# Optimization experiments

Measured on AMD Instinct MI355X. Metric: run time of the kernel, lower is better.

## Reference

```python
import jax, jax.numpy as jnp
import numpy as np

N_NODES = 100000


def _gcn_norm(edge_index, num_nodes):
    # add self loops, then symmetric normalization D^-1/2 (A+I) D^-1/2
    loops = jnp.arange(num_nodes, dtype=edge_index.dtype)
    src = jnp.concatenate([edge_index[0], loops])
    dst = jnp.concatenate([edge_index[1], loops])
    ones = jnp.ones(src.shape[0], dtype=jnp.float32)
    deg = jax.ops.segment_sum(ones, dst, num_segments=num_nodes)
    dinv = jnp.where(deg > 0, jax.lax.rsqrt(deg), 0.0)
    norm = dinv[src] * dinv[dst]  # [E+N]
    return src, dst, norm


def setup_inputs() -> dict:
    key = jax.random.key(0)
    k1, k2, k3, k4 = jax.random.split(key, 4)
    x = jax.random.normal(k1, (N_NODES, 512), dtype=jnp.float32)
    edge_index = jax.random.randint(k2, (2, 3200000), 0, N_NODES, dtype=jnp.int64)
    # SGConv linear: Linear(num_features=512, num_classes=40)
    W = jax.random.normal(k3, (40, 512), dtype=jnp.float32) / np.sqrt(512.0)
    b = jax.random.normal(k4, (40,), dtype=jnp.float32) * 0.01
    return {"x": x, "edge_index": edge_index, "W": W, "b": b}


def reference(x, edge_index, W, b):
    K = 2  # args.num_layers
    src, dst, norm = _gcn_norm(edge_index, N_NODES)
    h = x
    for _ in range(K):
        # SpMM: out[dst] += norm * h[src]
        h = jax.ops.segment_sum(norm[:, None] * h[src], dst, num_segments=N_NODES)
    logits = h @ W.T + b  # [N, num_classes]
    return jax.nn.log_softmax(logits, axis=1)
```

## Files before the change

### kernel.cpp

```cpp
#include <hip/hip_runtime.h>
#include <hip/hip_bf16.h>
#include <math.h>


#define NFEAT 512
#define NCLS  40
#define NBUCK_MAX 512
#define CAP   9728

typedef __attribute__((ext_vector_type(8))) short bf16x8;
typedef __attribute__((ext_vector_type(4))) float f32x4;

__device__ inline short f2bf(float f) {
    union { float f; unsigned u; } v; v.f = f;
    unsigned r = (v.u + 0x7FFFu + ((v.u >> 16) & 1u)) >> 16;
    return (short)r;
}
__device__ inline float bf2f(unsigned short u) {
    union { unsigned u; float f; } r; r.u = (unsigned)u << 16; return r.f;
}


__global__ __launch_bounds__(256) void scat7_kernel(const int* __restrict__ src,
                                                    const int* __restrict__ dst,
                                                    int* __restrict__ bcursor,
                                                    unsigned* __restrict__ bco, int E) {
    __shared__ int h[NBUCK_MAX], h2[NBUCK_MAX], base[NBUCK_MAX];
    int t = threadIdx.x;
    h[t] = 0; h[t + 256] = 0; h2[t] = 0; h2[t + 256] = 0;
    __syncthreads();
    int cb = blockIdx.x * 2048;
    int d[8], s[8];
    bool m[8];
    #pragma unroll
    for (int u = 0; u < 8; ++u) {
        int e = cb + u * 256 + t;
        m[u] = e < E;
        d[u] = m[u] ? __builtin_nontemporal_load(dst + e) : 0;
        s[u] = m[u] ? __builtin_nontemporal_load(src + e) : 0;
        if (m[u]) atomicAdd(&h[d[u] >> 8], 1);
    }
    __syncthreads();
    #pragma unroll
    for (int b = 0; b < 2; ++b) {
        int bb = t + b * 256;
        if (h[bb]) base[bb] = bb * CAP + atomicAdd(&bcursor[bb], h[bb]);
    }
    __syncthreads();
    #pragma unroll
    for (int u = 0; u < 8; ++u) {
        if (m[u]) {
            int b = d[u] >> 8;
            int lp = atomicAdd(&h2[b], 1);
            bco[base[b] + lp] = ((unsigned)s[u] << 8) | (unsigned)(d[u] & 255);
        }
    }
}


__global__ __launch_bounds__(256) void sortb3_kernel(const unsigned* __restrict__ bco,
                                                     const int* __restrict__ bcursor,
                                                     int4* __restrict__ rowinfo,
                                                     float* __restrict__ dinv,
                                                     int* __restrict__ csr_src, int N) {
    __shared__ int deg[256], ex[256], sc[256];
    int b = blockIdx.x, t = threadIdx.x;
    int lo = b * 256;
    int nn = N - lo; if (nn > 256) nn = 256;
    int ebeg = b * CAP;
    int ecnt = bcursor[b];

    deg[t] = 0;
    __syncthreads();
    for (int i = t; i < ecnt; i += 256)
        atomicAdd(&deg[bco[ebeg + i] & 255u], 1);
    __syncthreads();
    int v = deg[t];
    sc[t] = v;
    __syncthreads();
    for (int off = 1; off < 256; off <<= 1) {
        int u = (t >= off) ? sc[t - off] : 0;
        __syncthreads();
        sc[t] += u;
        __syncthreads();
    }
    int ext = sc[t] - v;
    ex[t] = ext;
    if (t < nn) {
        float di = rsqrtf((float)(v + 1));
        int4 ri;
        ri.x = ebeg + ext;
        ri.y = v;
        ri.z = __float_as_int(di);
        ri.w = 0;
        rowinfo[lo + t] = ri;
        dinv[lo + t]    = di;
    }
    __syncthreads();
    for (int i = t; i < ecnt; i += 256) {
        unsigned e = bco[ebeg + i];
        int p = atomicAdd(&ex[e & 255u], 1);
        csr_src[ebeg + p] = (int)(e >> 8);
    }
}


__global__ void wfrag_kernel(const float* __restrict__ W, short* __restrict__ wfrag) {
    int i = blockIdx.x * blockDim.x + threadIdx.x;
    if (i >= 16 * 3 * 64) return;
    int kc = i / 192, rem = i % 192, tile = rem / 64, lane = rem % 64;
    int c = tile * 16 + (lane & 15);
    int kbase = kc * 32 + ((lane >> 4) << 3);
    bf16x8 out;
    #pragma unroll
    for (int j = 0; j < 8; ++j) {
        float v = (c < NCLS) ? W[(size_t)c * NFEAT + kbase + j] : 0.f;
        out[j] = f2bf(v);
    }
    *(bf16x8*)(wfrag + (size_t)i * 8) = out;
}


__global__ __launch_bounds__(512) void gemm5_kernel(const float* __restrict__ x,
                                                    const short* __restrict__ wfrag,
                                                    const float* __restrict__ dinv,
                                                    unsigned short* __restrict__ zb, int n) {
    __shared__ short xl[2][128 * 40];
    int t = threadIdx.x;
    int w = t >> 6, l = t & 63;
    int lrow = l & 15, lk = l >> 4;
    int rowBase = blockIdx.x * 128;
    int srow = t >> 2, skq = t & 3;
    f32x4 acc0 = {0.f, 0.f, 0.f, 0.f}, acc1 = acc0, acc2 = acc0;
    const float* xrow = x + (size_t)(rowBase + srow) * NFEAT + skq * 8;
    bool srOK = (rowBase + srow) < n;
    int aoff = (w * 16 + lrow) * 40 + lk * 8;
    int doff = srow * 40 + skq * 8;

    {
        float4 v0 = make_float4(0.f, 0.f, 0.f, 0.f), v1 = v0;
        if (srOK) { const float4* xp = (const float4*)xrow; v0 = xp[0]; v1 = xp[1]; }
        bf16x8 bv;
        bv[0] = f2bf(v0.x); bv[1] = f2bf(v0.y); bv[2] = f2bf(v0.z); bv[3] = f2bf(v0.w);
        bv[4] = f2bf(v1.x); bv[5] = f2bf(v1.y); bv[6] = f2bf(v1.z); bv[7] = f2bf(v1.w);
        *(bf16x8*)&xl[0][doff] = bv;
    }
    __syncthreads();

    for (int kc = 0; kc < 16; ++kc) {
        int cur = kc & 1;
        float4 v0 = make_float4(0.f, 0.f, 0.f, 0.f), v1 = v0;
        if (kc < 15 && srOK) {
            const float4* xp = (const float4*)(xrow + (kc + 1) * 32);
            v0 = xp[0]; v1 = xp[1];
        }
        bf16x8 af = *(const bf16x8*)&xl[cur][aoff];
        const bf16x8* wf = (const bf16x8*)(wfrag + (size_t)kc * 3 * 64 * 8);
        bf16x8 b0 = wf[l];
        bf16x8 b1 = wf[64 + l];
        bf16x8 b2 = wf[128 + l];
        acc0 = __builtin_amdgcn_mfma_f32_16x16x32_bf16(af, b0, acc0, 0, 0, 0);
        acc1 = __builtin_amdgcn_mfma_f32_16x16x32_bf16(af, b1, acc1, 0, 0, 0);
        acc2 = __builtin_amdgcn_mfma_f32_16x16x32_bf16(af, b2, acc2, 0, 0, 0);
        if (kc < 15) {
            bf16x8 bv;
            bv[0] = f2bf(v0.x); bv[1] = f2bf(v0.y); bv[2] = f2bf(v0.z); bv[3] = f2bf(v0.w);
            bv[4] = f2bf(v1.x); bv[5] = f2bf(v1.y); bv[6] = f2bf(v1.z); bv[7] = f2bf(v1.w);
            *(bf16x8*)&xl[cur ^ 1][doff] = bv;
            __syncthreads();
        }
    }
    int r0 = rowBase + w * 16 + lk * 4;
    #pragma unroll
    for (int reg = 0; reg < 4; ++reg) {
        int row = r0 + reg;
        if (row < n) {
            float sc = dinv[row];
            unsigned short* zp = zb + (size_t)row * NCLS;
            zp[lrow]      = (unsigned short)f2bf(acc0[reg] * sc);
            zp[16 + lrow] = (unsigned short)f2bf(acc1[reg] * sc);
            if (lrow < 8) zp[32 + lrow] = (unsigned short)f2bf(acc2[reg] * sc);
        }
    }
}


template <bool FINAL>
__global__ __launch_bounds__(256) void spmm6_kernel(const unsigned short* __restrict__ in,
                                                    const int4* __restrict__ rowinfo,
                                                    const int* __restrict__ csr,
                                                    const float* __restrict__ bias,
                                                    void* __restrict__ outv, int n) {
    int wv = (int)((blockIdx.x * (size_t)blockDim.x + threadIdx.x) >> 6);
    wv = __builtin_amdgcn_readfirstlane(wv);
    if (wv >= n) return;
    int lane = threadIdx.x & 63;
    bool lact = lane < NCLS;

    int4 ri = rowinfo[wv];
    int beg = ri.x, tot = ri.y;
    float dd = __int_as_float(ri.z);

    float a = lact ? bf2f(in[(size_t)wv * NCLS + lane]) : 0.f;

    int j = 0;
    for (; j + 4 <= tot; j += 4) {
        int s0 = csr[beg + j];
        int s1 = csr[beg + j + 1];
        int s2 = csr[beg + j + 2];
        int s3 = csr[beg + j + 3];
        if (lact) {
            float v0 = bf2f(in[(size_t)s0 * NCLS + lane]);
            float v1 = bf2f(in[(size_t)s1 * NCLS + lane]);
            float v2 = bf2f(in[(size_t)s2 * NCLS + lane]);
            float v3 = bf2f(in[(size_t)s3 * NCLS + lane]);
            a += v0; a += v1; a += v2; a += v3;
        }
    }
    for (; j < tot; ++j) {
        int s = csr[beg + j];
        if (lact) a += bf2f(in[(size_t)s * NCLS + lane]);
    }

    if (!FINAL) {
        if (lact) {
            unsigned short* ob = (unsigned short*)outv;
            ob[(size_t)wv * NCLS + lane] = (unsigned short)f2bf(a * dd * dd);
        }
    } else {
        float v = lact ? a * dd + bias[lane] : -INFINITY;
        float m = v;
        #pragma unroll
        for (int off = 32; off; off >>= 1) m = fmaxf(m, __shfl_xor(m, off, 64));
        float e = lact ? expf(v - m) : 0.f;
        float s = e;
        #pragma unroll
        for (int off = 32; off; off >>= 1) s += __shfl_xor(s, off, 64);
        float lse = logf(s);
        if (lact) {
            float* out = (float*)outv;
            out[(size_t)wv * NCLS + lane] = v - m - lse;
        }
    }
}


extern "C" void kernel_launch(void* const* d_in, const int* in_sizes, int n_in,
                              void* d_out, int out_size, void* d_ws, size_t ws_size,
                              hipStream_t stream) {
    const float* x  = (const float*)d_in[0];
    const int*   ei = (const int*)d_in[1];
    const float* W  = (const float*)d_in[2];
    const float* b  = (const float*)d_in[3];

    const int N = in_sizes[0] / NFEAT;
    const int E = in_sizes[1] / 2;
    const int* src = ei;
    const int* dst = ei + E;
    const int nbuck = (N + 255) >> 8;

    char* p = (char*)d_ws;
    auto alloc = [&](size_t bytes) -> void* {
        void* r = (void*)p;
        p += (bytes + 255) & ~(size_t)255;
        return r;
    };
    int*      bcursor = (int*)     alloc((size_t)NBUCK_MAX * 4);
    int4*     rowinfo = (int4*)    alloc((size_t)N * 16);
    float*    dinv    = (float*)   alloc((size_t)N * 4);
    unsigned* bco     = (unsigned*)alloc((size_t)nbuck * CAP * 4 + 64);
    int*      csr_src = (int*)     alloc((size_t)nbuck * CAP * 4 + 64);
    short*    wfrag   = (short*)   alloc((size_t)16 * 3 * 64 * 8 * 2);
    unsigned short* zb = (unsigned short*)alloc((size_t)N * NCLS * 2 + 256);
    unsigned short* h1 = (unsigned short*)alloc((size_t)N * NCLS * 2 + 256);

    hipMemsetAsync(bcursor, 0, (size_t)NBUCK_MAX * 4, stream);

    int cb = (E + 2047) / 2048;
    scat7_kernel<<<cb, 256, 0, stream>>>(src, dst, bcursor, bco, E);
    sortb3_kernel<<<nbuck, 256, 0, stream>>>(bco, bcursor, rowinfo, dinv, csr_src, N);

    wfrag_kernel<<<12, 256, 0, stream>>>(W, wfrag);
    gemm5_kernel<<<(N + 127) / 128, 512, 0, stream>>>(x, wfrag, dinv, zb, N);

    int wb = (int)(((size_t)N * 64 + 255) / 256);
    spmm6_kernel<false><<<wb, 256, 0, stream>>>(zb, rowinfo, csr_src, b, h1, N);
    spmm6_kernel<true ><<<wb, 256, 0, stream>>>(h1, rowinfo, csr_src, b, d_out, N);
}
```

Baseline: 294.9 us.

## Pad features to 64 bf16 and gather 8 neighbors per wave with 16-byte loads

Intermediate feature rows are padded from 40 to 64 bf16 so that each row is 128 bytes. The SpMM kernel now assigns 8 lanes per neighbor row, each loading 16 bytes, so one wave gathers 8 neighbors at a time. Partial sums are combined with cross-lane shuffles and the log-softmax runs over packed lanes. The hipMemset is folded into the wfrag kernel, which now runs first. The change trades 60% more gather bytes from padding for fewer, wider memory transactions and more neighbors in flight per wave.

```diff
diff --git a/kernel.cpp b/kernel.cpp
--- a/kernel.cpp
+++ b/kernel.cpp
@@ -16,8 +16,14 @@
     unsigned r = (v.u + 0x7FFFu + ((v.u >> 16) & 1u)) >> 16;
     return (short)r;
 }
-__device__ inline float bf2f(unsigned short u) {
-    union { unsigned u; float f; } r; r.u = (unsigned)u << 16; return r.f;
+__device__ inline unsigned pack2bf(float a, float b) {
+    return (unsigned)(unsigned short)f2bf(a) | ((unsigned)(unsigned short)f2bf(b) << 16);
+}
+__device__ inline float bflo(unsigned v) {
+    union { unsigned u; float f; } r; r.u = v << 16; return r.f;
+}
+__device__ inline float bfhi(unsigned v) {
+    union { unsigned u; float f; } r; r.u = v & 0xFFFF0000u; return r.f;
 }
 
 
@@ -105,8 +111,10 @@
 }
 
 
-__global__ void wfrag_kernel(const float* __restrict__ W, short* __restrict__ wfrag) {
+__global__ void wfrag_kernel(const float* __restrict__ W, short* __restrict__ wfrag,
+                             int* __restrict__ bcursor) {
     int i = blockIdx.x * blockDim.x + threadIdx.x;
+    if (i < NBUCK_MAX) bcursor[i] = 0;
     if (i >= 16 * 3 * 64) return;
     int kc = i / 192, rem = i % 192, tile = rem / 64, lane = rem % 64;
     int c = tile * 16 + (lane & 15);
@@ -121,10 +129,10 @@
 }
 
 
-__global__ __launch_bounds__(512) void gemm5_kernel(const float* __restrict__ x,
+__global__ __launch_bounds__(512) void gemm7_kernel(const float* __restrict__ x,
                                                     const short* __restrict__ wfrag,
                                                     const float* __restrict__ dinv,
-                                                    unsigned short* __restrict__ zb, int n) {
+                                                    unsigned short* __restrict__ zp, int n) {
     __shared__ short xl[2][128 * 40];
     int t = threadIdx.x;
     int w = t >> 6, l = t & 63;
@@ -176,70 +184,123 @@
         int row = r0 + reg;
         if (row < n) {
             float sc = dinv[row];
-            unsigned short* zp = zb + (size_t)row * NCLS;
-            zp[lrow]      = (unsigned short)f2bf(acc0[reg] * sc);
-            zp[16 + lrow] = (unsigned short)f2bf(acc1[reg] * sc);
-            if (lrow < 8) zp[32 + lrow] = (unsigned short)f2bf(acc2[reg] * sc);
+            unsigned short* zr = zp + (size_t)row * 64;
+            zr[lrow]      = (unsigned short)f2bf(acc0[reg] * sc);
+            zr[16 + lrow] = (unsigned short)f2bf(acc1[reg] * sc);
+            zr[32 + lrow] = (lrow < 8) ? (unsigned short)f2bf(acc2[reg] * sc) : 0;
+            zr[48 + lrow] = 0;
         }
     }
 }
 
 
 template <bool FINAL>
-__global__ __launch_bounds__(256) void spmm6_kernel(const unsigned short* __restrict__ in,
-                                                    const int4* __restrict__ rowinfo,
-                                                    const int* __restrict__ csr,
-                                                    const float* __restrict__ bias,
-                                                    void* __restrict__ outv, int n) {
+__global__ __launch_bounds__(256) void spmm12_kernel(const unsigned short* __restrict__ in,
+                                                     const int4* __restrict__ rowinfo,
+                                                     const int* __restrict__ csr,
+                                                     const float* __restrict__ bias,
+                                                     unsigned short* __restrict__ outP,
+                                                     float* __restrict__ outF, int n) {
     int wv = (int)((blockIdx.x * (size_t)blockDim.x + threadIdx.x) >> 6);
     wv = __builtin_amdgcn_readfirstlane(wv);
     if (wv >= n) return;
     int lane = threadIdx.x & 63;
-    bool lact = lane < NCLS;
+    int g  = lane >> 3;
+    int oc = lane & 7;
+
+    const char* rowb = (const char*)in + oc * 16;
 
     int4 ri = rowinfo[wv];
     int beg = ri.x, tot = ri.y;
     float dd = __int_as_float(ri.z);
 
-    float a = lact ? bf2f(in[(size_t)wv * NCLS + lane]) : 0.f;
+    float a0 = 0.f, a1 = 0.f, a2 = 0.f, a3 = 0.f,
+          a4 = 0.f, a5 = 0.f, a6 = 0.f, a7 = 0.f;
+
+#define ACC_ADD(V)                                                     \
+    { a0 += bflo((V).x); a1 += bfhi((V).x); a2 += bflo((V).y);         \
+      a3 += bfhi((V).y); a4 += bflo((V).z); a5 += bfhi((V).z);         \
+      a6 += bflo((V).w); a7 += bfhi((V).w); }
+
+    if (g == 0) {
+        uint4 v = *(const uint4*)(rowb + (size_t)wv * 128);
+        ACC_ADD(v);
+    }
 
     int j = 0;
-    for (; j + 4 <= tot; j += 4) {
-        int s0 = csr[beg + j];
-        int s1 = csr[beg + j + 1];
-        int s2 = csr[beg + j + 2];
-        int s3 = csr[beg + j + 3];
-        if (lact) {
-            float v0 = bf2f(in[(size_t)s0 * NCLS + lane]);
-            float v1 = bf2f(in[(size_t)s1 * NCLS + lane]);
-            float v2 = bf2f(in[(size_t)s2 * NCLS + lane]);
-            float v3 = bf2f(in[(size_t)s3 * NCLS + lane]);
-            a += v0; a += v1; a += v2; a += v3;
-        }
-    }
-    for (; j < tot; ++j) {
-        int s = csr[beg + j];
-        if (lact) a += bf2f(in[(size_t)s * NCLS + lane]);
+    for (; j + 32 <= tot; j += 32) {
+        int s0 = csr[beg + j + g];
+        int s1 = csr[beg + j + 8 + g];
+        int s2 = csr[beg + j + 16 + g];
+        int s3 = csr[beg + j + 24 + g];
+        uint4 v0 = *(const uint4*)(rowb + (size_t)s0 * 128);
+        uint4 v1 = *(const uint4*)(rowb + (size_t)s1 * 128);
+        uint4 v2 = *(const uint4*)(rowb + (size_t)s2 * 128);
+        uint4 v3 = *(const uint4*)(rowb + (size_t)s3 * 128);
+        ACC_ADD(v0); ACC_ADD(v1); ACC_ADD(v2); ACC_ADD(v3);
+    }
+    for (; j < tot; j += 8) {
+        if (g < tot - j) {
+            int s = csr[beg + j + g];
+            uint4 v = *(const uint4*)(rowb + (size_t)s * 128);
+            ACC_ADD(v);
+        }
+    }
+#undef ACC_ADD
+
+    #pragma unroll
+    for (int off = 8; off <= 32; off <<= 1) {
+        a0 += __shfl_xor(a0, off, 64); a1 += __shfl_xor(a1, off, 64);
+        a2 += __shfl_xor(a2, off, 64); a3 += __shfl_xor(a3, off, 64);
+        a4 += __shfl_xor(a4, off, 64); a5 += __shfl_xor(a5, off, 64);
+        a6 += __shfl_xor(a6, off, 64); a7 += __shfl_xor(a7, off, 64);
     }
 
     if (!FINAL) {
-        if (lact) {
-            unsigned short* ob = (unsigned short*)outv;
-            ob[(size_t)wv * NCLS + lane] = (unsigned short)f2bf(a * dd * dd);
+        if (g == 0) {
+            float s2 = dd * dd;
+            uint4 o;
+            o.x = pack2bf(a0 * s2, a1 * s2);
+            o.y = pack2bf(a2 * s2, a3 * s2);
+            o.z = pack2bf(a4 * s2, a5 * s2);
+            o.w = pack2bf(a6 * s2, a7 * s2);
+            *(uint4*)((char*)outP + (size_t)wv * 128 + oc * 16) = o;
         }
     } else {
-        float v = lact ? a * dd + bias[lane] : -INFINITY;
-        float m = v;
+        float b0 = 0.f, b1 = 0.f, b2 = 0.f, b3 = 0.f,
+              b4 = 0.f, b5 = 0.f, b6 = 0.f, b7 = 0.f;
+        if (oc < 5) {
+            float4 q0 = ((const float4*)bias)[oc * 2];
+            float4 q1 = ((const float4*)bias)[oc * 2 + 1];
+            b0 = q0.x; b1 = q0.y; b2 = q0.z; b3 = q0.w;
+            b4 = q1.x; b5 = q1.y; b6 = q1.z; b7 = q1.w;
+        }
+        bool valid = oc < 5;
+        float v0 = valid ? a0 * dd + b0 : -INFINITY;
+        float v1 = valid ? a1 * dd + b1 : -INFINITY;
+        float v2 = valid ? a2 * dd + b2 : -INFINITY;
+        float v3 = valid ? a3 * dd + b3 : -INFINITY;
+        float v4 = valid ? a4 * dd + b4 : -INFINITY;
+        float v5 = valid ? a5 * dd + b5 : -INFINITY;
+        float v6 = valid ? a6 * dd + b6 : -INFINITY;
+        float v7 = valid ? a7 * dd + b7 : -INFINITY;
+        float m = fmaxf(fmaxf(fmaxf(v0, v1), fmaxf(v2, v3)),
+                        fmaxf(fmaxf(v4, v5), fmaxf(v6, v7)));
         #pragma unroll
-        for (int off = 32; off; off >>= 1) m = fmaxf(m, __shfl_xor(m, off, 64));
-        float e = lact ? expf(v - m) : 0.f;
-        float s = e;
+        for (int off = 1; off <= 4; off <<= 1) m = fmaxf(m, __shfl_xor(m, off, 64));
+        float es = 0.f;
+        if (valid)
+            es = expf(v0 - m) + expf(v1 - m) + expf(v2 - m) + expf(v3 - m)
+               + expf(v4 - m) + expf(v5 - m) + expf(v6 - m) + expf(v7 - m);
         #pragma unroll
-        for (int off = 32; off; off >>= 1) s += __shfl_xor(s, off, 64);
-        float lse = logf(s);
-        if (lact) {
-            float* out = (float*)outv;
-            out[(size_t)wv * NCLS + lane] = v - m - lse;
+        for (int off = 1; off <= 4; off <<= 1) es += __shfl_xor(es, off, 64);
+        float lse = logf(es) + m;
+        if (g == 0 && valid) {
+            float* op = outF + (size_t)wv * NCLS + oc * 8;
+            float4 o0 = make_float4(v0 - lse, v1 - lse, v2 - lse, v3 - lse);
+            float4 o1 = make_float4(v4 - lse, v5 - lse, v6 - lse, v7 - lse);
+            *(float4*)op = o0;
+            *(float4*)(op + 4) = o1;
         }
     }
 }
@@ -271,19 +332,19 @@
     unsigned* bco     = (unsigned*)alloc((size_t)nbuck * CAP * 4 + 64);
     int*      csr_src = (int*)     alloc((size_t)nbuck * CAP * 4 + 64);
     short*    wfrag   = (short*)   alloc((size_t)16 * 3 * 64 * 8 * 2);
-    unsigned short* zb = (unsigned short*)alloc((size_t)N * NCLS * 2 + 256);
-    unsigned short* h1 = (unsigned short*)alloc((size_t)N * NCLS * 2 + 256);
-
-    hipMemsetAsync(bcursor, 0, (size_t)NBUCK_MAX * 4, stream);
+    unsigned short* zp  = (unsigned short*)alloc((size_t)N * 64 * 2);
+    unsigned short* h1p = (unsigned short*)alloc((size_t)N * 64 * 2);
+
+    wfrag_kernel<<<12, 256, 0, stream>>>(W, wfrag, bcursor);
 
     int cb = (E + 2047) / 2048;
     scat7_kernel<<<cb, 256, 0, stream>>>(src, dst, bcursor, bco, E);
     sortb3_kernel<<<nbuck, 256, 0, stream>>>(bco, bcursor, rowinfo, dinv, csr_src, N);
 
-    wfrag_kernel<<<12, 256, 0, stream>>>(W, wfrag);
-    gemm5_kernel<<<(N + 127) / 128, 512, 0, stream>>>(x, wfrag, dinv, zb, N);
+    gemm7_kernel<<<(N + 127) / 128, 512, 0, stream>>>(x, wfrag, dinv, zp, N);
 
     int wb = (int)(((size_t)N * 64 + 255) / 256);
-    spmm6_kernel<false><<<wb, 256, 0, stream>>>(zb, rowinfo, csr_src, b, h1, N);
-    spmm6_kernel<true ><<<wb, 256, 0, stream>>>(h1, rowinfo, csr_src, b, d_out, N);
-}
+    spmm12_kernel<false><<<wb, 256, 0, stream>>>(zp, rowinfo, csr_src, b, h1p, nullptr, N);
+    spmm12_kernel<true ><<<wb, 256, 0, stream>>>(h1p, rowinfo, csr_src, b, nullptr,
+                                                 (float*)d_out, N);
+}
```

Result: faster. 259.1 us (median of 2 runs) (-12.1%).
